# Performance work log

Hardware: AMD Instinct MI355X
Metric: run time of the kernel (lower is better)

## Reference

```python
import jax, jax.numpy as jnp
import numpy as np

B, T, C, H = 4, 2048, 1024, 16
D = C // H  # head_dim = 64


def setup_inputs() -> dict:
    key = jax.random.key(0)
    k1, k2, k3, k4, k5 = jax.random.split(key, 5)
    x = jax.random.normal(k1, (B, T, C), jnp.float32)
    w_qkv = jax.random.normal(k2, (3 * C, C), jnp.float32) * 0.02
    w_proj = jax.random.normal(k3, (C, C), jnp.float32) * 0.02
    b_proj = jax.random.normal(k4, (C,), jnp.float32) * 0.02
    # torch.randperm(T): a fixed random permutation of the keys
    perm = jax.random.permutation(k5, T).astype(jnp.int32)
    return {"x": x, "w_qkv": w_qkv, "w_proj": w_proj, "b_proj": b_proj, "perm": perm}


def reference(x, w_qkv, w_proj, b_proj, perm):
    Bx, Tx, Cx = x.shape
    # QKV projection (no bias), split into heads: (B, H, T, D)
    qkv = (x @ w_qkv.T).reshape(Bx, Tx, 3, H, D)
    q, k, v = jnp.moveaxis(qkv, 2, 0)            # each (B, T, H, D)
    q = q.transpose(0, 2, 1, 3)                   # (B, H, T, D)
    k = k.transpose(0, 2, 1, 3)
    v = v.transpose(0, 2, 1, 3)
    scale = 1.0 / np.float32(np.sqrt(D))
    scores = jnp.einsum('bhqd,bhkd->bhqk', q, k) * scale  # (B, H, T, T)
    # permuted causal mask: query i may attend to key j iff perm[j] <= i
    allowed = perm[None, :] <= jnp.arange(Tx)[:, None]     # (T, T) bool
    scores = jnp.where(allowed[None, None], scores, -jnp.inf)
    att = jax.nn.softmax(scores, axis=-1)
    y = jnp.einsum('bhqk,bhkd->bhqd', att, v)              # (B, H, T, D)
    y = y.transpose(0, 2, 1, 3).reshape(Bx, Tx, Cx)        # (B, T, C)
    return y @ w_proj.T + b_proj
```

## Files before the change

kernel.cpp:

```cpp
#include <hip/hip_runtime.h>
#include <stdint.h>

#define T_   2048
#define NH   16
#define HD   64
#define NBH  64
#define CDIM 1024
#define MROWS 8192

typedef __attribute__((ext_vector_type(8))) short short8;
typedef __attribute__((ext_vector_type(4))) float f32x4;
typedef __attribute__((ext_vector_type(16))) float f32x16;
typedef __attribute__((ext_vector_type(2))) unsigned int uint32x2;

#define LOG2E 1.44269504088896340736f

static __device__ __forceinline__ uint16_t f2bf(float f) {
  uint32_t u = __float_as_uint(f);
  return (uint16_t)((u + 0x7FFFu + ((u >> 16) & 1u)) >> 16);
}

static __device__ __forceinline__ void async16(const void* g, void* l) {
  __builtin_amdgcn_global_load_lds(
      (const __attribute__((address_space(1))) uint32_t*)g,
      (__attribute__((address_space(3))) uint32_t*)l, 16, 0, 0);
}

static __device__ __forceinline__ uint32x2 plswap(uint32_t a, uint32_t b) {
  return __builtin_amdgcn_permlane32_swap(a, b, false, false);
}
static __device__ __forceinline__ float halves_max(float x) {
  uint32x2 r = plswap(__float_as_uint(x), __float_as_uint(x));
  return fmaxf(__uint_as_float(r[0]), __uint_as_float(r[1]));
}
static __device__ __forceinline__ float halves_sum(float x) {
  uint32x2 r = plswap(__float_as_uint(x), __float_as_uint(x));
  return __uint_as_float(r[0]) + __uint_as_float(r[1]);
}
static __device__ __forceinline__ uint32_t pkbf(float lo, float hi) {
  uint32_t r;
  asm("v_cvt_pk_bf16_f32 %0, %1, %2" : "=v"(r) : "v"(lo), "v"(hi));
  return r;
}
static __device__ __forceinline__ float tmax32(const f32x16& a, const f32x16& b) {
  float t[16];
#pragma unroll
  for (int r = 0; r < 16; ++r) t[r] = fmaxf(a[r], b[r]);
#pragma unroll
  for (int s = 8; s >= 1; s >>= 1)
#pragma unroll
    for (int r = 0; r < s; ++r) t[r] = fmaxf(t[r], t[r + s]);
  return t[0];
}
static __device__ __forceinline__ float tsum32(const f32x16& a, const f32x16& b) {
  float t[16];
#pragma unroll
  for (int r = 0; r < 16; ++r) t[r] = a[r] + b[r];
#pragma unroll
  for (int s = 8; s >= 1; s >>= 1)
#pragma unroll
    for (int r = 0; r < s; ++r) t[r] += t[r + s];
  return t[0];
}

__global__ __launch_bounds__(256) void cvt_f32_bf16(const float* __restrict__ in,
                                                    uint16_t* __restrict__ out, int n) {
  int i = (blockIdx.x * 256 + threadIdx.x) * 4;
  int stride = gridDim.x * 256 * 4;
  for (; i < n; i += stride) {
    float4 v = *(const float4*)(in + i);
    ushort4 o;
    o.x = f2bf(v.x); o.y = f2bf(v.y); o.z = f2bf(v.z); o.w = f2bf(v.w);
    *(ushort4*)(out + i) = o;
  }
}

template <int MODE>
__global__ __launch_bounds__(256) void gemm_bt(
    const uint16_t* __restrict__ A, const uint16_t* __restrict__ Bt,
    float* __restrict__ Cout, const float* __restrict__ bias,
    uint16_t* __restrict__ Qo, uint16_t* __restrict__ Ko, uint16_t* __restrict__ Vo,
    const int* __restrict__ perm, int N) {
  __shared__ uint16_t lA[128 * 32];
  __shared__ uint16_t lB[128 * 32];

  const int t = threadIdx.x;
  const int lane = t & 63, wv = t >> 6;
  const int gq = lane >> 4, lc = lane & 15;
  const int mbase = blockIdx.x * 128;
  const int nbase = blockIdx.y * 128;
  const int wr = (wv >> 1) * 64, wc = (wv & 1) * 64;

  f32x4 acc[4][4];
#pragma unroll
  for (int i = 0; i < 4; ++i)
#pragma unroll
    for (int j = 0; j < 4; ++j) acc[i][j] = (f32x4){0.f, 0.f, 0.f, 0.f};

  const int srow = t >> 2;
  const int scb  = (t & 3) * 16;

  for (int kt = 0; kt < 32; ++kt) {
    const char* baseA = (const char*)A + ((size_t)mbase * CDIM + kt * 32) * 2;
    const char* baseB = (const char*)Bt + ((size_t)nbase * CDIM + kt * 32) * 2;
#pragma unroll
    for (int j = 0; j < 2; ++j) {
      int row = j * 64 + srow;
      async16(baseA + (size_t)row * (CDIM * 2) + scb, (char*)lA + j * 4096 + wv * 1024);
    }
#pragma unroll
    for (int j = 0; j < 2; ++j) {
      int row = j * 64 + srow;
      async16(baseB + (size_t)row * (CDIM * 2) + scb, (char*)lB + j * 4096 + wv * 1024);
    }
    asm volatile("s_waitcnt vmcnt(0)" ::: "memory");
    __syncthreads();

    short8 af[4], bfr[4];
#pragma unroll
    for (int mi = 0; mi < 4; ++mi)
      af[mi] = *(const short8*)&lA[(wr + mi * 16 + lc) * 32 + 8 * gq];
#pragma unroll
    for (int ni = 0; ni < 4; ++ni)
      bfr[ni] = *(const short8*)&lB[(wc + ni * 16 + lc) * 32 + 8 * gq];
#pragma unroll
    for (int mi = 0; mi < 4; ++mi)
#pragma unroll
      for (int ni = 0; ni < 4; ++ni)
        acc[mi][ni] = __builtin_amdgcn_mfma_f32_16x16x32_bf16(af[mi], bfr[ni], acc[mi][ni], 0, 0, 0);
    __syncthreads();
  }

  if (MODE == 0) {
#pragma unroll
    for (int mi = 0; mi < 4; ++mi) {
      int row = mbase + wr + mi * 16 + 4 * gq;
#pragma unroll
      for (int ni = 0; ni < 4; ++ni) {
        int col = nbase + wc + ni * 16 + lc;
        float bv = bias[col];
#pragma unroll
        for (int r = 0; r < 4; ++r)
          Cout[(size_t)(row + r) * N + col] = acc[mi][ni][r] + bv;
      }
    }
  } else {
#pragma unroll
    for (int mi = 0; mi < 4; ++mi) {
#pragma unroll
      for (int r = 0; r < 4; ++r) {
        int m = mbase + wr + mi * 16 + 4 * gq + r;
        int b = m >> 11, s = m & 2047;
        int p = perm[s];
#pragma unroll
        for (int ni = 0; ni < 4; ++ni) {
          int col = nbase + wc + ni * 16 + lc;
          int typ = col >> 10, cc = col & 1023;
          int h = cc >> 6, d = cc & 63;
          int bh = b * 16 + h;
          float v = acc[mi][ni][r];
          if (typ == 0)
            Qo[((size_t)bh * T_ + s) * HD + d] = f2bf(v * (0.125f * LOG2E));
          else if (typ == 1)
            Ko[((size_t)bh * T_ + p) * HD + d] = f2bf(v);
          else
            Vo[((size_t)bh * T_ + p) * HD + d] = f2bf(v);
        }
      }
    }
  }
}

__global__ __launch_bounds__(256) void transpose_v(const uint16_t* __restrict__ Vp,
                                                   uint16_t* __restrict__ Vt) {
  __shared__ uint16_t tile[64][72];
  const int pb = blockIdx.x * 64;
  const int bh = blockIdx.y;
  const int t = threadIdx.x;
  const uint16_t* src = Vp + (size_t)bh * T_ * HD + (size_t)pb * HD;
#pragma unroll
  for (int it = 0; it < 2; ++it) {
    int lin = it * 256 + t;
    int row = lin >> 3, col = (lin & 7) * 8;
    short8 v = *(const short8*)(src + row * HD + col);
    *(short8*)&tile[row][col] = v;
  }
  __syncthreads();
  uint16_t* dst = Vt + (size_t)bh * HD * T_;
#pragma unroll
  for (int it = 0; it < 2; ++it) {
    int lin = it * 256 + t;
    int d = lin >> 3, ps = (lin & 7) * 8;
    short8 v;
#pragma unroll
    for (int j = 0; j < 8; ++j) v[j] = (short)tile[ps + j][d];
    *(short8*)(dst + (size_t)d * T_ + pb + ps) = v;
  }
}

__global__ __launch_bounds__(256, 4) void attn_kernel(
    const uint16_t* __restrict__ Q, const uint16_t* __restrict__ Kp,
    const uint16_t* __restrict__ Vt, uint16_t* __restrict__ Y) {
  __shared__ __attribute__((aligned(16))) uint16_t lK[2][64 * 64];
  __shared__ __attribute__((aligned(16))) uint16_t lV[2][64 * 64];

  const int bh = blockIdx.x;
  const int b = bh >> 4, h = bh & 15;
  const int qb = (gridDim.y - 1 - blockIdx.y) * 128;
  const int t = threadIdx.x;
  const int lane = t & 63, wv = t >> 6;
  const int l31 = lane & 31, hi = lane >> 5;
  const int qw = qb + 32 * wv;
  const int qg = qw + l31;

  const uint16_t* Qb = Q + ((size_t)bh * T_ + qw) * HD;
  const uint16_t* Kb = Kp + (size_t)bh * T_ * HD;
  const uint16_t* Vb = Vt + (size_t)bh * HD * T_;

  const int srow8 = lane >> 3;
  const int schunk = (lane & 7) ^ srow8;

  short8 qf[4];
#pragma unroll
  for (int kc = 0; kc < 4; ++kc)
    qf[kc] = *(const short8*)(Qb + (size_t)l31 * HD + 16 * kc + 8 * hi);

  f32x16 ot[2];
#pragma unroll
  for (int dt = 0; dt < 2; ++dt)
#pragma unroll
    for (int r = 0; r < 16; ++r) ot[dt][r] = 0.f;
  float mrun = -__builtin_inff();
  float lrun = 0.f;

  const int nkt_blk = (qb >> 6) + 2;
  const int myKt = qw >> 6;

  {
    const int p0 = 0;
#pragma unroll
    for (int j = 0; j < 2; ++j) {
      int i = 2 * wv + j;
      async16(Kb + (size_t)(p0 + 8 * i + srow8) * HD + schunk * 8,
              (char*)&lK[0][0] + i * 1024);
      async16(Vb + (size_t)(8 * i + srow8) * T_ + p0 + schunk * 8,
              (char*)&lV[0][0] + i * 1024);
    }
  }

  const int swz = (l31 & 7);

  for (int kt = 0; kt < nkt_blk; ++kt) {
    const int cur = kt & 1;
    const int p0 = kt * 64;
    if (kt + 1 < nkt_blk) {
      const int pn = p0 + 64;
#pragma unroll
      for (int j = 0; j < 2; ++j) {
        int i = 2 * wv + j;
        async16(Kb + (size_t)(pn + 8 * i + srow8) * HD + schunk * 8,
                (char*)&lK[cur ^ 1][0] + i * 1024);
        async16(Vb + (size_t)(8 * i + srow8) * T_ + pn + schunk * 8,
                (char*)&lV[cur ^ 1][0] + i * 1024);
      }
      asm volatile("s_waitcnt vmcnt(4)" ::: "memory");
    } else {
      asm volatile("s_waitcnt vmcnt(0)" ::: "memory");
    }
    __syncthreads();

    if (kt <= myKt) {
      const uint16_t* lk = &lK[cur][0];
      const uint16_t* lv = &lV[cur][0];

      f32x16 st[2];
#pragma unroll
      for (int a = 0; a < 2; ++a) {
        short8 kf[4];
#pragma unroll
        for (int kc = 0; kc < 4; ++kc)
          kf[kc] = *(const short8*)&lk[(32 * a + l31) * 64 + (((2 * kc + hi) ^ swz) * 8)];
#pragma unroll
        for (int r = 0; r < 16; ++r) st[a][r] = 0.f;
        __builtin_amdgcn_s_setprio(1);
#pragma unroll
        for (int kc = 0; kc < 4; ++kc)
          st[a] = __builtin_amdgcn_mfma_f32_32x32x16_bf16(kf[kc], qf[kc], st[a], 0, 0, 0);
        __builtin_amdgcn_s_setprio(0);
      }

      if (kt == myKt) {
#pragma unroll
        for (int a = 0; a < 2; ++a) {
          int kbase = p0 + 32 * a + 4 * hi;
#pragma unroll
          for (int r = 0; r < 16; ++r) {
            int key = kbase + (r & 3) + 8 * (r >> 2);
            if (key > qg) st[a][r] = -__builtin_inff();
          }
        }
      }

      float mall = halves_max(tmax32(st[0], st[1]));
      if (__any(mall > mrun + 8.0f)) {
        float mnew = fmaxf(mrun, mall);
        float alpha = __builtin_amdgcn_exp2f(mrun - mnew);
        mrun = mnew;
        lrun *= alpha;
#pragma unroll
        for (int dt = 0; dt < 2; ++dt)
#pragma unroll
          for (int r = 0; r < 16; ++r) ot[dt][r] *= alpha;
      }

#pragma unroll
      for (int a = 0; a < 2; ++a)
#pragma unroll
        for (int r = 0; r < 16; ++r)
          st[a][r] = __builtin_amdgcn_exp2f(st[a][r] - mrun);

      lrun += halves_sum(tsum32(st[0], st[1]));

      short8 pb[4];
#pragma unroll
      for (int kc = 0; kc < 4; ++kc) {
#define PV_(i) ((8 * kc + (i)) < 16 ? st[0][(8 * kc + (i)) & 15] : st[1][(8 * kc + (i)) & 15])
        uint32_t u0 = pkbf(PV_(0), PV_(1));
        uint32_t u1 = pkbf(PV_(2), PV_(3));
        uint32_t u2 = pkbf(PV_(4), PV_(5));
        uint32_t u3 = pkbf(PV_(6), PV_(7));
#undef PV_
        uint32x2 s02 = plswap(u0, u2);
        uint32x2 s13 = plswap(u1, u3);
        union { uint32_t w[4]; short8 s; } pbu;
        pbu.w[0] = s02[0]; pbu.w[1] = s13[0]; pbu.w[2] = s02[1]; pbu.w[3] = s13[1];
        pb[kc] = pbu.s;
      }

#pragma unroll
      for (int dt = 0; dt < 2; ++dt) {
        short8 vf[4];
#pragma unroll
        for (int kc = 0; kc < 4; ++kc)
          vf[kc] = *(const short8*)&lv[(32 * dt + l31) * 64 + (((2 * kc + hi) ^ swz) * 8)];
        __builtin_amdgcn_s_setprio(1);
#pragma unroll
        for (int kc = 0; kc < 4; ++kc)
          ot[dt] = __builtin_amdgcn_mfma_f32_32x32x16_bf16(vf[kc], pb[kc], ot[dt], 0, 0, 0);
        __builtin_amdgcn_s_setprio(0);
      }
    }
    __syncthreads();
  }

  float inv = 1.0f / lrun;
  uint16_t* Yrow = Y + ((size_t)b * T_ + qg) * CDIM + h * HD;
#pragma unroll
  for (int dt = 0; dt < 2; ++dt)
#pragma unroll
    for (int g = 0; g < 4; ++g) {
      int d0 = 32 * dt + 8 * g + 4 * hi;
      ushort4 o4;
      o4.x = f2bf(ot[dt][4 * g + 0] * inv);
      o4.y = f2bf(ot[dt][4 * g + 1] * inv);
      o4.z = f2bf(ot[dt][4 * g + 2] * inv);
      o4.w = f2bf(ot[dt][4 * g + 3] * inv);
      *(ushort4*)(Yrow + d0) = o4;
    }
}

extern "C" void kernel_launch(void* const* d_in, const int* in_sizes, int n_in,
                              void* d_out, int out_size, void* d_ws, size_t ws_size,
                              hipStream_t stream) {
  const float* x = (const float*)d_in[0];
  const float* wqkv = (const float*)d_in[1];
  const float* wproj = (const float*)d_in[2];
  const float* bproj = (const float*)d_in[3];
  const int* perm = (const int*)d_in[4];
  float* out = (float*)d_out;

  char* ws = (char*)d_ws;
  uint16_t* xb     = (uint16_t*)(ws + 0);
  uint16_t* wqkvb  = (uint16_t*)(ws + 16777216);
  uint16_t* wprojb = (uint16_t*)(ws + 23068672);
  uint16_t* Qb     = (uint16_t*)(ws + 25165824);
  uint16_t* Kb     = (uint16_t*)(ws + 41943040);
  uint16_t* Vpb    = (uint16_t*)(ws + 58720256);
  uint16_t* Vtb    = (uint16_t*)(ws + 75497472);
  uint16_t* Yb     = xb;

  cvt_f32_bf16<<<2048, 256, 0, stream>>>(x, xb, MROWS * CDIM);
  cvt_f32_bf16<<<1024, 256, 0, stream>>>(wqkv, wqkvb, 3 * CDIM * CDIM);
  cvt_f32_bf16<<<512, 256, 0, stream>>>(wproj, wprojb, CDIM * CDIM);

  gemm_bt<1><<<dim3(64, 24), 256, 0, stream>>>(xb, wqkvb, nullptr, nullptr,
                                               Qb, Kb, Vpb, perm, 3072);
  transpose_v<<<dim3(32, 64), 256, 0, stream>>>(Vpb, Vtb);
  attn_kernel<<<dim3(64, 16), 256, 0, stream>>>(Qb, Kb, Vtb, Yb);
  gemm_bt<0><<<dim3(64, 8), 256, 0, stream>>>(Yb, wprojb, out, bproj,
                                              nullptr, nullptr, nullptr, nullptr, CDIM);
}
```

Measured before the change: 177.4 us.

## Replace QKV GEMM with 256x256 tiled, 4-stage async-pipelined kernel

Adds a dedicated QKV projection kernel that uses 256x256 output tiles with 8 waves per block. It loads through a 4-deep ring of LDS buffers using direct global-to-LDS async loads with a staggered vmcnt wait, and applies an XOR swizzle to avoid LDS bank conflicts. It also remaps block IDs for L2 locality and raises wave priority around the MFMA bursts. The goal is to hide global load latency and raise arithmetic intensity over the old 128x128 single-buffered GEMM. The cost is 64KB of LDS per block and heavy register use, which may limit occupancy.

```diff
diff --git a/kernel.cpp b/kernel.cpp
--- a/kernel.cpp
+++ b/kernel.cpp
@@ -75,12 +75,137 @@
   }
 }
 
-template <int MODE>
+__global__ __launch_bounds__(512, 2) void gemm256_qkv(
+    const uint16_t* __restrict__ A, const uint16_t* __restrict__ Bt,
+    uint16_t* __restrict__ Qo, uint16_t* __restrict__ Ko, uint16_t* __restrict__ Vo,
+    const int* __restrict__ perm) {
+  __shared__ __attribute__((aligned(16))) uint16_t lA[4][256 * 32];
+  __shared__ __attribute__((aligned(16))) uint16_t lB[4][256 * 32];
+
+  const int orig = blockIdx.x;
+  const int wgid = (orig & 7) * 48 + (orig >> 3);
+  const int bx = wgid & 31;
+  const int by = wgid >> 5;
+  const int mbase = bx * 256, nbase = by * 256;
+
+  const int t = threadIdx.x;
+  const int lane = t & 63, wv = t >> 6;
+  const int wm = wv >> 2, wn = wv & 3;
+  const int gq = lane >> 4, lc = lane & 15;
+
+  const int srow = lane >> 2;
+  const int scs = (lane & 3) ^ (srow & 3);
+
+  f32x4 acc[8][4];
+#pragma unroll
+  for (int i = 0; i < 8; ++i)
+#pragma unroll
+    for (int j = 0; j < 4; ++j) acc[i][j] = (f32x4){0.f, 0.f, 0.f, 0.f};
+
+  const int rxor = (lc & 3);
+
+#pragma unroll
+  for (int k0 = 0; k0 < 3; ++k0) {
+#pragma unroll
+    for (int j = 0; j < 2; ++j) {
+      int row = 32 * wv + 16 * j;
+      async16(A + ((size_t)(mbase + row + srow) * CDIM + k0 * 32 + scs * 8),
+              (char*)&lA[k0][row * 32]);
+      async16(Bt + ((size_t)(nbase + row + srow) * CDIM + k0 * 32 + scs * 8),
+              (char*)&lB[k0][row * 32]);
+    }
+  }
+  asm volatile("s_waitcnt vmcnt(8)" ::: "memory");
+  __builtin_amdgcn_s_barrier();
+
+  for (int kt = 0; kt < 32; ++kt) {
+    const uint16_t* pa = &lA[kt & 3][0];
+    const uint16_t* pb = &lB[kt & 3][0];
+    const int ks = kt + 3;
+
+    if (ks < 32) {
+#pragma unroll
+      for (int j = 0; j < 2; ++j) {
+        int row = 32 * wv + 16 * j;
+        async16(A + ((size_t)(mbase + row + srow) * CDIM + ks * 32 + scs * 8),
+                (char*)&lA[ks & 3][row * 32]);
+      }
+    }
+    short8 bfr[4], af[4];
+#pragma unroll
+    for (int ni = 0; ni < 4; ++ni)
+      bfr[ni] = *(const short8*)&pb[(wn * 64 + ni * 16 + lc) * 32 + ((gq ^ rxor) * 8)];
+#pragma unroll
+    for (int mi = 0; mi < 4; ++mi)
+      af[mi] = *(const short8*)&pa[(wm * 128 + mi * 16 + lc) * 32 + ((gq ^ rxor) * 8)];
+    __builtin_amdgcn_s_setprio(1);
+#pragma unroll
+    for (int mi = 0; mi < 4; ++mi)
+#pragma unroll
+      for (int ni = 0; ni < 4; ++ni)
+        acc[mi][ni] = __builtin_amdgcn_mfma_f32_16x16x32_bf16(af[mi], bfr[ni], acc[mi][ni], 0, 0, 0);
+    __builtin_amdgcn_s_setprio(0);
+
+    if (ks < 32) {
+#pragma unroll
+      for (int j = 0; j < 2; ++j) {
+        int row = 32 * wv + 16 * j;
+        async16(Bt + ((size_t)(nbase + row + srow) * CDIM + ks * 32 + scs * 8),
+                (char*)&lB[ks & 3][row * 32]);
+      }
+    }
+    short8 af2[4];
+#pragma unroll
+    for (int mi = 0; mi < 4; ++mi)
+      af2[mi] = *(const short8*)&pa[(wm * 128 + (mi + 4) * 16 + lc) * 32 + ((gq ^ rxor) * 8)];
+    __builtin_amdgcn_s_setprio(1);
+#pragma unroll
+    for (int mi = 0; mi < 4; ++mi)
+#pragma unroll
+      for (int ni = 0; ni < 4; ++ni)
+        acc[mi + 4][ni] = __builtin_amdgcn_mfma_f32_16x16x32_bf16(af2[mi], bfr[ni], acc[mi + 4][ni], 0, 0, 0);
+    __builtin_amdgcn_s_setprio(0);
+
+    if (kt < 29) {
+      asm volatile("s_waitcnt vmcnt(8)" ::: "memory");
+      __builtin_amdgcn_s_barrier();
+    } else if (kt == 29) {
+      asm volatile("s_waitcnt vmcnt(4)" ::: "memory");
+      __builtin_amdgcn_s_barrier();
+    } else if (kt == 30) {
+      asm volatile("s_waitcnt vmcnt(0)" ::: "memory");
+      __builtin_amdgcn_s_barrier();
+    }
+  }
+
+#pragma unroll
+  for (int mi = 0; mi < 8; ++mi) {
+#pragma unroll
+    for (int rr = 0; rr < 4; ++rr) {
+      int m = mbase + wm * 128 + mi * 16 + 4 * gq + rr;
+      int b = m >> 11, s = m & 2047;
+      int p = perm[s];
+#pragma unroll
+      for (int ni = 0; ni < 4; ++ni) {
+        int col = nbase + wn * 64 + ni * 16 + lc;
+        int typ = col >> 10, cc = col & 1023;
+        int h = cc >> 6, d = cc & 63;
+        int bh = b * 16 + h;
+        float v = acc[mi][ni][rr];
+        if (typ == 0)
+          Qo[((size_t)bh * T_ + s) * HD + d] = f2bf(v * (0.125f * LOG2E));
+        else if (typ == 1)
+          Ko[((size_t)bh * T_ + p) * HD + d] = f2bf(v);
+        else
+          Vo[((size_t)bh * T_ + p) * HD + d] = f2bf(v);
+      }
+    }
+  }
+}
+
 __global__ __launch_bounds__(256) void gemm_bt(
     const uint16_t* __restrict__ A, const uint16_t* __restrict__ Bt,
-    float* __restrict__ Cout, const float* __restrict__ bias,
-    uint16_t* __restrict__ Qo, uint16_t* __restrict__ Ko, uint16_t* __restrict__ Vo,
-    const int* __restrict__ perm, int N) {
+    float* __restrict__ Cout, const float* __restrict__ bias, int N) {
   __shared__ uint16_t lA[128 * 32];
   __shared__ uint16_t lB[128 * 32];
 
@@ -131,42 +256,16 @@
     __syncthreads();
   }
 
-  if (MODE == 0) {
-#pragma unroll
-    for (int mi = 0; mi < 4; ++mi) {
-      int row = mbase + wr + mi * 16 + 4 * gq;
-#pragma unroll
-      for (int ni = 0; ni < 4; ++ni) {
-        int col = nbase + wc + ni * 16 + lc;
-        float bv = bias[col];
-#pragma unroll
-        for (int r = 0; r < 4; ++r)
-          Cout[(size_t)(row + r) * N + col] = acc[mi][ni][r] + bv;
-      }
-    }
-  } else {
-#pragma unroll
-    for (int mi = 0; mi < 4; ++mi) {
-#pragma unroll
-      for (int r = 0; r < 4; ++r) {
-        int m = mbase + wr + mi * 16 + 4 * gq + r;
-        int b = m >> 11, s = m & 2047;
-        int p = perm[s];
-#pragma unroll
-        for (int ni = 0; ni < 4; ++ni) {
-          int col = nbase + wc + ni * 16 + lc;
-          int typ = col >> 10, cc = col & 1023;
-          int h = cc >> 6, d = cc & 63;
-          int bh = b * 16 + h;
-          float v = acc[mi][ni][r];
-          if (typ == 0)
-            Qo[((size_t)bh * T_ + s) * HD + d] = f2bf(v * (0.125f * LOG2E));
-          else if (typ == 1)
-            Ko[((size_t)bh * T_ + p) * HD + d] = f2bf(v);
-          else
-            Vo[((size_t)bh * T_ + p) * HD + d] = f2bf(v);
-        }
-      }
+#pragma unroll
+  for (int mi = 0; mi < 4; ++mi) {
+    int row = mbase + wr + mi * 16 + 4 * gq;
+#pragma unroll
+    for (int ni = 0; ni < 4; ++ni) {
+      int col = nbase + wc + ni * 16 + lc;
+      float bv = bias[col];
+#pragma unroll
+      for (int r = 0; r < 4; ++r)
+        Cout[(size_t)(row + r) * N + col] = acc[mi][ni][r] + bv;
     }
   }
 }
@@ -393,10 +492,8 @@
   cvt_f32_bf16<<<1024, 256, 0, stream>>>(wqkv, wqkvb, 3 * CDIM * CDIM);
   cvt_f32_bf16<<<512, 256, 0, stream>>>(wproj, wprojb, CDIM * CDIM);
 
-  gemm_bt<1><<<dim3(64, 24), 256, 0, stream>>>(xb, wqkvb, nullptr, nullptr,
-                                               Qb, Kb, Vpb, perm, 3072);
+  gemm256_qkv<<<384, 512, 0, stream>>>(xb, wqkvb, Qb, Kb, Vpb, perm);
   transpose_v<<<dim3(32, 64), 256, 0, stream>>>(Vpb, Vtb);
   attn_kernel<<<dim3(64, 16), 256, 0, stream>>>(Qb, Kb, Vtb, Yb);
-  gemm_bt<0><<<dim3(64, 8), 256, 0, stream>>>(Yb, wprojb, out, bproj,
-                                              nullptr, nullptr, nullptr, nullptr, CDIM);
-}
+  gemm_bt<<<dim3(64, 8), 256, 0, stream>>>(Yb, wprojb, out, bproj, CDIM);
+}
```

After: 212.3 us. +19.7%, slower.

## Merge the three bf16 conversion launches and XOR-swizzle GEMM LDS tiles

Applied to the files above, without the earlier changes.

The three separate f32-to-bf16 conversion kernels are merged into one launch that walks the three arrays in turn, removing two kernel launches. The GEMM's LDS staging now stores each row's 16-byte chunks at an XOR-permuted column index, and the fragment reads apply the matching XOR. This is meant to cut LDS bank conflicts on the short8 fragment reads. The risk is that the swizzle on the write side (keyed on thread bits) and on the read side (keyed on lc) do not pair up, which would give wrong results.

```diff
diff --git a/kernel.cpp b/kernel.cpp
--- a/kernel.cpp
+++ b/kernel.cpp
@@ -63,15 +63,25 @@
   return t[0];
 }
 
-__global__ __launch_bounds__(256) void cvt_f32_bf16(const float* __restrict__ in,
-                                                    uint16_t* __restrict__ out, int n) {
-  int i = (blockIdx.x * 256 + threadIdx.x) * 4;
-  int stride = gridDim.x * 256 * 4;
-  for (; i < n; i += stride) {
-    float4 v = *(const float4*)(in + i);
-    ushort4 o;
-    o.x = f2bf(v.x); o.y = f2bf(v.y); o.z = f2bf(v.z); o.w = f2bf(v.w);
-    *(ushort4*)(out + i) = o;
+__global__ __launch_bounds__(256) void cvt3_f32_bf16(
+    const float* __restrict__ a, uint16_t* __restrict__ oa, int na,
+    const float* __restrict__ b, uint16_t* __restrict__ ob, int nb,
+    const float* __restrict__ c, uint16_t* __restrict__ oc, int nc) {
+  const int stride = gridDim.x * 256 * 4;
+  for (int i = (blockIdx.x * 256 + threadIdx.x) * 4; i < na; i += stride) {
+    float4 v = *(const float4*)(a + i);
+    ushort4 o; o.x = f2bf(v.x); o.y = f2bf(v.y); o.z = f2bf(v.z); o.w = f2bf(v.w);
+    *(ushort4*)(oa + i) = o;
+  }
+  for (int i = (blockIdx.x * 256 + threadIdx.x) * 4; i < nb; i += stride) {
+    float4 v = *(const float4*)(b + i);
+    ushort4 o; o.x = f2bf(v.x); o.y = f2bf(v.y); o.z = f2bf(v.z); o.w = f2bf(v.w);
+    *(ushort4*)(ob + i) = o;
+  }
+  for (int i = (blockIdx.x * 256 + threadIdx.x) * 4; i < nc; i += stride) {
+    float4 v = *(const float4*)(c + i);
+    ushort4 o; o.x = f2bf(v.x); o.y = f2bf(v.y); o.z = f2bf(v.z); o.w = f2bf(v.w);
+    *(ushort4*)(oc + i) = o;
   }
 }
 
@@ -98,7 +108,8 @@
     for (int j = 0; j < 4; ++j) acc[i][j] = (f32x4){0.f, 0.f, 0.f, 0.f};
 
   const int srow = t >> 2;
-  const int scb  = (t & 3) * 16;
+  const int scb  = (((t & 3) ^ ((t >> 3) & 3)) * 16);
+  const int rxs  = (lc >> 1) & 3;
 
   for (int kt = 0; kt < 32; ++kt) {
     const char* baseA = (const char*)A + ((size_t)mbase * CDIM + kt * 32) * 2;
@@ -119,10 +130,10 @@
     short8 af[4], bfr[4];
 #pragma unroll
     for (int mi = 0; mi < 4; ++mi)
-      af[mi] = *(const short8*)&lA[(wr + mi * 16 + lc) * 32 + 8 * gq];
+      af[mi] = *(const short8*)&lA[(wr + mi * 16 + lc) * 32 + ((gq ^ rxs) * 8)];
 #pragma unroll
     for (int ni = 0; ni < 4; ++ni)
-      bfr[ni] = *(const short8*)&lB[(wc + ni * 16 + lc) * 32 + 8 * gq];
+      bfr[ni] = *(const short8*)&lB[(wc + ni * 16 + lc) * 32 + ((gq ^ rxs) * 8)];
 #pragma unroll
     for (int mi = 0; mi < 4; ++mi)
 #pragma unroll
@@ -389,9 +400,9 @@
   uint16_t* Vtb    = (uint16_t*)(ws + 75497472);
   uint16_t* Yb     = xb;
 
-  cvt_f32_bf16<<<2048, 256, 0, stream>>>(x, xb, MROWS * CDIM);
-  cvt_f32_bf16<<<1024, 256, 0, stream>>>(wqkv, wqkvb, 3 * CDIM * CDIM);
-  cvt_f32_bf16<<<512, 256, 0, stream>>>(wproj, wprojb, CDIM * CDIM);
+  cvt3_f32_bf16<<<2048, 256, 0, stream>>>(x, xb, MROWS * CDIM,
+                                          wqkv, wqkvb, 3 * CDIM * CDIM,
+                                          wproj, wprojb, CDIM * CDIM);
 
   gemm_bt<1><<<dim3(64, 24), 256, 0, stream>>>(xb, wqkvb, nullptr, nullptr,
                                                Qb, Kb, Vpb, perm, 3072);
```

Measured after the change: 170.8 us. 1.04x faster.
